# Kernel optimization log

Hardware: AMD Instinct MI355X
Metric: run time of the kernel (lower is better)

Reference implementation:

```python
import jax, jax.numpy as jnp
import numpy as np

# Qwen3-0.6B-like config; 4 equal-length requests flattened into [R*S, H]
L, R, S, H = 2, 4, 1024, 1024
NH, NKV, DH = 16, 8, 128
FF = 3072
EPS = 1e-6
THETA = 1e6
SCALE = 0.02  # weight init scale to keep activations sane


def setup_inputs() -> dict:
    key = jax.random.key(0)
    ks = jax.random.split(key, 8)
    return {
        "hidden_states": jax.random.normal(ks[0], (R * S, H), jnp.float32),
        "Wq": jax.random.normal(ks[1], (L, H, NH * DH), jnp.float32) * SCALE,
        "Wk": jax.random.normal(ks[2], (L, H, NKV * DH), jnp.float32) * SCALE,
        "Wv": jax.random.normal(ks[3], (L, H, NKV * DH), jnp.float32) * SCALE,
        "Wo": jax.random.normal(ks[4], (L, NH * DH, H), jnp.float32) * SCALE,
        "q_norm_w": jnp.ones((L, DH), jnp.float32),
        "k_norm_w": jnp.ones((L, DH), jnp.float32),
        "ln1_w": jnp.ones((L, H), jnp.float32),
        "ln2_w": jnp.ones((L, H), jnp.float32),
        "Wg": jax.random.normal(ks[5], (L, H, FF), jnp.float32) * SCALE,
        "Wu": jax.random.normal(ks[6], (L, H, FF), jnp.float32) * SCALE,
        "Wd": jax.random.normal(ks[7], (L, FF, H), jnp.float32) * SCALE,
        "final_norm_w": jnp.ones((H,), jnp.float32),
    }


def _rms(x, w):
    return x * jax.lax.rsqrt(jnp.mean(x * x, axis=-1, keepdims=True) + EPS) * w


def _rope_tables():
    inv_freq = 1.0 / (THETA ** (jnp.arange(0, DH, 2, dtype=jnp.float32) / DH))
    pos = jnp.arange(S, dtype=jnp.float32)  # per-request positions 0..S-1 (prefill)
    freqs = pos[:, None] * inv_freq[None, :]        # [S, DH/2]
    emb = jnp.concatenate([freqs, freqs], axis=-1)  # [S, DH]
    return jnp.cos(emb), jnp.sin(emb)


def _rotate_half(x):
    x1, x2 = jnp.split(x, 2, axis=-1)
    return jnp.concatenate([-x2, x1], axis=-1)


def _apply_rope(x, cos, sin):
    # x: [R, heads, S, DH]; cos/sin: [S, DH]
    c = cos[None, None]
    s = sin[None, None]
    return x * c + _rotate_half(x) * s


def reference(hidden_states, Wq, Wk, Wv, Wo, q_norm_w, k_norm_w, ln1_w, ln2_w,
              Wg, Wu, Wd, final_norm_w):
    cos, sin = _rope_tables()
    causal = jnp.tril(jnp.ones((S, S), dtype=bool))  # per-request causal mask
    neg = jnp.finfo(hidden_states.dtype).min
    scaling = 1.0 / jnp.sqrt(jnp.asarray(DH, hidden_states.dtype))

    x = hidden_states
    for l in range(L):
        # --- attention block ---
        residual = x
        h = _rms(x, ln1_w[l])                       # [R*S, H]
        q = (h @ Wq[l]).reshape(R, S, NH, DH)
        k = (h @ Wk[l]).reshape(R, S, NKV, DH)
        v = (h @ Wv[l]).reshape(R, S, NKV, DH)
        q = _rms(q, q_norm_w[l]).transpose(0, 2, 1, 3)   # [R, NH, S, DH]
        k = _rms(k, k_norm_w[l]).transpose(0, 2, 1, 3)   # [R, NKV, S, DH]
        v = v.transpose(0, 2, 1, 3)                      # [R, NKV, S, DH]
        q = _apply_rope(q, cos, sin)
        k = _apply_rope(k, cos, sin)
        # GQA: repeat KV heads
        rep = NH // NKV
        k = jnp.repeat(k, rep, axis=1)
        v = jnp.repeat(v, rep, axis=1)
        scores = jnp.einsum('rhqd,rhkd->rhqk', q, k) * scaling
        scores = jnp.where(causal[None, None], scores, neg)
        attn = jax.nn.softmax(scores, axis=-1)
        o = jnp.einsum('rhqk,rhkd->rhqd', attn, v)       # [R, NH, S, DH]
        o = o.transpose(0, 2, 1, 3).reshape(R * S, NH * DH)
        x = residual + o @ Wo[l]
        # --- MLP block ---
        residual = x
        h = _rms(x, ln2_w[l])
        x = residual + (jax.nn.silu(h @ Wg[l]) * (h @ Wu[l])) @ Wd[l]
    return _rms(x, final_norm_w)
```

## Files before the change

### kernel.cpp

```cpp
#include <hip/hip_runtime.h>
#include <hip/hip_bf16.h>

typedef __bf16 bf16;
typedef __bf16 bf16x8 __attribute__((ext_vector_type(8)));
typedef float f32x4 __attribute__((ext_vector_type(4)));

#define DEVINL __device__ __forceinline__

constexpr int L_ = 2, R_ = 4, S_ = 1024, H_ = 1024;
constexpr int NH_ = 16, NKV_ = 8, DH_ = 128;
constexpr int FF_ = 3072;
constexpr int T_ = R_ * S_;

DEVINL void gload16(const bf16* g, bf16* l) {
    __builtin_amdgcn_global_load_lds(
        (const __attribute__((address_space(1))) void*)g,
        (__attribute__((address_space(3))) void*)l, 16, 0, 0);
}

__global__ void rope_tables_kernel(float* __restrict__ cosb, float* __restrict__ sinb) {
    int s = blockIdx.x;
    int i = threadIdx.x;
    float inv = __expf(-(float)i * (1.0f / 64.0f) * 13.815510557964274f);
    float f = (float)s * inv;
    cosb[s * 64 + i] = cosf(f);
    sinb[s * 64 + i] = sinf(f);
}

template <bool OUT_BF16>
__global__ __launch_bounds__(256) void rmsnorm_kernel(const float* __restrict__ x,
                                                      const float* __restrict__ w,
                                                      void* __restrict__ out) {
    int row = blockIdx.x;
    const float* xr = x + (size_t)row * H_;
    int t = threadIdx.x;
    float v[4];
    float ss = 0.f;
#pragma unroll
    for (int j = 0; j < 4; ++j) {
        v[j] = xr[t + 256 * j];
        ss += v[j] * v[j];
    }
#pragma unroll
    for (int off = 32; off; off >>= 1) ss += __shfl_xor(ss, off);
    __shared__ float part[4];
    if ((t & 63) == 0) part[t >> 6] = ss;
    __syncthreads();
    ss = part[0] + part[1] + part[2] + part[3];
    float r = rsqrtf(ss * (1.0f / (float)H_) + 1e-6f);
#pragma unroll
    for (int j = 0; j < 4; ++j) {
        int c = t + 256 * j;
        float o = v[j] * r * w[c];
        if constexpr (OUT_BF16)
            ((bf16*)out)[(size_t)row * H_ + c] = (bf16)o;
        else
            ((float*)out)[(size_t)row * H_ + c] = o;
    }
}

__global__ __launch_bounds__(256) void transpose_cast_kernel(const float* __restrict__ in,
                                                             bf16* __restrict__ out,
                                                             int Rk, int Cn, int mode) {
    __shared__ float tile[32][33];
    int c0 = blockIdx.x * 32, r0 = blockIdx.y * 32;
    int t = threadIdx.x;
    int tc = t & 31, tr = t >> 5;
#pragma unroll
    for (int i = 0; i < 4; ++i) {
        int r = tr + i * 8;
        tile[r][tc] = in[(size_t)(r0 + r) * Cn + c0 + tc];
    }
    __syncthreads();
#pragma unroll
    for (int i = 0; i < 4; ++i) {
        int c = c0 + tr + i * 8;
        int n = (mode == 0) ? c : (((c >> 4) << 5) + ((mode == 2) ? 16 : 0) + (c & 15));
        out[(size_t)n * Rk + r0 + tc] = (bf16)tile[tc][tr + i * 8];
    }
}

__global__ __launch_bounds__(256) void vt_kernel(const bf16* __restrict__ qkv,
                                                 bf16* __restrict__ vt) {
    __shared__ bf16 tile[32][34];
    int s0 = blockIdx.x * 32, c0 = blockIdx.y * 32, r = blockIdx.z;
    int t = threadIdx.x, tc = t & 31, tr = t >> 5;
#pragma unroll
    for (int i = 0; i < 4; ++i) {
        int s = tr + i * 8;
        tile[s][tc] = qkv[(size_t)(r * 1024 + s0 + s) * 4096 + 3072 + c0 + tc];
    }
    __syncthreads();
#pragma unroll
    for (int i = 0; i < 4; ++i) {
        int c = tr + i * 8;
        vt[((size_t)(r * 1024 + c0 + c)) * 1024 + s0 + tc] = tile[tc][c];
    }
}

template <int EPI>
__global__ __launch_bounds__(512, 2) void gemmQ_kernel(const bf16* __restrict__ A,
                                                       const bf16* __restrict__ Bt,
                                                       void* __restrict__ out,
                                                       int M, int N, int K) {
    __shared__ bf16 lds[49152];
    const int NT = K >> 5;
    int nbm = M >> 8, nbn = N >> 8;
    int slice = nbn >> 3;
    int id = blockIdx.x;
    int xcd = id & 7, wi = id >> 3;
    int bm = (wi % nbm) << 8, bn = (xcd * slice + wi / nbm) << 8;
    int t = threadIdx.x, lane = t & 63, w = t >> 6;
    int wm = w >> 2, wn = w & 3;
    int hi = lane >> 4, f = lane & 15;

    int srow = t >> 2;
    int ssc = (t & 3) ^ ((srow >> 1) & 3);
    const bf16* a0 = A + (size_t)(bm + srow) * K + (ssc << 3);
    const bf16* a1 = A + (size_t)(bm + 128 + srow) * K + (ssc << 3);
    const bf16* b0 = Bt + (size_t)(bn + srow) * K + (ssc << 3);
    const bf16* b1 = Bt + (size_t)(bn + 128 + srow) * K + (ssc << 3);

    f32x4 acc[8][4] = {};

    auto stage = [&](int tt, int sb) {
        gload16(a0 + tt * 32, lds + sb * 8192 + w * 512);
        gload16(a1 + tt * 32, lds + sb * 8192 + 4096 + w * 512);
        gload16(b0 + tt * 32, lds + 24576 + sb * 8192 + w * 512);
        gload16(b1 + tt * 32, lds + 24576 + sb * 8192 + 4096 + w * 512);
    };

    stage(0, 0);
    stage(1, 1);
    asm volatile("s_waitcnt vmcnt(4)" ::: "memory");
    __builtin_amdgcn_s_barrier();

    int cb = 0;
    for (int tau = 0; tau < NT; ++tau) {
        const bf16* aB = lds + cb * 8192;
        const bf16* bB = lds + 24576 + cb * 8192;
        if (tau + 2 < NT) stage(tau + 2, (cb == 0) ? 2 : cb - 1);
        bf16x8 af[8], bfv[4];
#pragma unroll
        for (int mf = 0; mf < 8; ++mf) {
            int row = wm * 128 + mf * 16 + f;
            af[mf] = *(const bf16x8*)(aB + row * 32 + ((hi ^ ((row >> 1) & 3)) << 3));
        }
#pragma unroll
        for (int nf = 0; nf < 4; ++nf) {
            int row = wn * 64 + nf * 16 + f;
            bfv[nf] = *(const bf16x8*)(bB + row * 32 + ((hi ^ ((row >> 1) & 3)) << 3));
        }
        __builtin_amdgcn_s_setprio(1);
#pragma unroll
        for (int mf = 0; mf < 8; ++mf)
#pragma unroll
            for (int nf = 0; nf < 4; ++nf)
                acc[mf][nf] = __builtin_amdgcn_mfma_f32_16x16x32_bf16(af[mf], bfv[nf],
                                                                      acc[mf][nf], 0, 0, 0);
        __builtin_amdgcn_s_setprio(0);
        if (tau < NT - 2)
            asm volatile("s_waitcnt vmcnt(4)" ::: "memory");
        else
            asm volatile("s_waitcnt vmcnt(0)" ::: "memory");
        __builtin_amdgcn_s_barrier();
        cb = (cb == 2) ? 0 : cb + 1;
    }

    int rb = bm + wm * 128 + hi * 4;
    int cb2 = bn + wn * 64 + f;
#pragma unroll
    for (int mf = 0; mf < 8; ++mf)
#pragma unroll
        for (int nf = 0; nf < 4; ++nf)
#pragma unroll
            for (int g = 0; g < 4; ++g)
                ((bf16*)out)[(size_t)(rb + mf * 16 + g) * N + cb2 + nf * 16] =
                    (bf16)acc[mf][nf][g];
}

template <int EPI>
__global__ __launch_bounds__(512, 4) void gemmP_kernel(const bf16* __restrict__ A,
                                                       const bf16* __restrict__ Bt,
                                                       void* __restrict__ out,
                                                       int M, int N, int K) {
    __shared__ bf16 lds[36864];
    const int NT = K >> 5;
    int nbm = M >> 7, nbn = N >> 8;
    int slice = nbn >> 3;
    int id = blockIdx.x;
    int xcd = id & 7, wi = id >> 3;
    int bm = (wi % nbm) << 7, bn = (xcd * slice + wi / nbm) << 8;
    int t = threadIdx.x, lane = t & 63, w = t >> 6;
    int wm = w >> 2, wn = w & 3;
    int hi = lane >> 4, f = lane & 15;

    int srow = t >> 2;
    int ssc = (t & 3) ^ ((srow >> 1) & 3);
    const bf16* aSrc = A + (size_t)(bm + srow) * K + (ssc << 3);
    const bf16* b0Src = Bt + (size_t)(bn + srow) * K + (ssc << 3);
    const bf16* b1Src = Bt + (size_t)(bn + 128 + srow) * K + (ssc << 3);

    f32x4 acc[4][4] = {};

    auto stage = [&](int tt, int sb) {
        gload16(aSrc + tt * 32, lds + sb * 4096 + w * 512);
        gload16(b0Src + tt * 32, lds + 12288 + sb * 8192 + w * 512);
        gload16(b1Src + tt * 32, lds + 12288 + sb * 8192 + 4096 + w * 512);
    };

    stage(0, 0);
    stage(1, 1);
    asm volatile("s_waitcnt vmcnt(3)" ::: "memory");
    __builtin_amdgcn_s_barrier();

    int cb = 0;
    for (int tau = 0; tau < NT; ++tau) {
        const bf16* aB = lds + cb * 4096;
        const bf16* bB = lds + 12288 + cb * 8192;
        if (tau + 2 < NT) stage(tau + 2, (cb == 0) ? 2 : cb - 1);
        bf16x8 af[4], bfv[4];
#pragma unroll
        for (int mf = 0; mf < 4; ++mf) {
            int row = wm * 64 + mf * 16 + f;
            af[mf] = *(const bf16x8*)(aB + row * 32 + ((hi ^ ((row >> 1) & 3)) << 3));
        }
#pragma unroll
        for (int nf = 0; nf < 4; ++nf) {
            int row = wn * 64 + nf * 16 + f;
            bfv[nf] = *(const bf16x8*)(bB + row * 32 + ((hi ^ ((row >> 1) & 3)) << 3));
        }
        __builtin_amdgcn_s_setprio(1);
#pragma unroll
        for (int mf = 0; mf < 4; ++mf)
#pragma unroll
            for (int nf = 0; nf < 4; ++nf)
                acc[mf][nf] = __builtin_amdgcn_mfma_f32_16x16x32_bf16(af[mf], bfv[nf],
                                                                      acc[mf][nf], 0, 0, 0);
        __builtin_amdgcn_s_setprio(0);
        if (tau < NT - 2)
            asm volatile("s_waitcnt vmcnt(3)" ::: "memory");
        else
            asm volatile("s_waitcnt vmcnt(0)" ::: "memory");
        __builtin_amdgcn_s_barrier();
        cb = (cb == 2) ? 0 : cb + 1;
    }

    int rb = bm + wm * 64 + hi * 4;
#pragma unroll
    for (int mf = 0; mf < 4; ++mf) {
        if constexpr (EPI == 5) {
#pragma unroll
            for (int p = 0; p < 2; ++p) {
                int col = ((bn + wn * 64) >> 1) + p * 16 + f;
#pragma unroll
                for (int g = 0; g < 4; ++g) {
                    float gv = acc[mf][2 * p][g], uv = acc[mf][2 * p + 1][g];
                    float sv = gv / (1.0f + __expf(-gv));
                    ((bf16*)out)[(size_t)(rb + mf * 16 + g) * (N / 2) + col] = (bf16)(sv * uv);
                }
            }
        } else {
            int cb2 = bn + wn * 64 + f;
#pragma unroll
            for (int nf = 0; nf < 4; ++nf)
#pragma unroll
                for (int g = 0; g < 4; ++g)
                    ((bf16*)out)[(size_t)(rb + mf * 16 + g) * N + cb2 + nf * 16] =
                        (bf16)acc[mf][nf][g];
        }
    }
}

template <int EPI, int BM>
__global__ __launch_bounds__(256) void gemm_kernel(const bf16* __restrict__ A,
                                                   const bf16* __restrict__ Bt,
                                                   void* __restrict__ out,
                                                   const float* __restrict__ res,
                                                   int M, int N, int K) {
    constexpr int MF = BM / 32;
    __shared__ bf16 Al[BM * 32];
    __shared__ bf16 Bl[128 * 32];
    int gx = gridDim.x;
    int nbm = gridDim.y;
    int id = blockIdx.y * gx + blockIdx.x;
    int slice = gx >> 3;
    int xcd = id & 7, wi = id >> 3;
    int bm = (wi % nbm) * BM, bn = (xcd * slice + wi / nbm) * 128;
    int t = threadIdx.x;
    int lane = t & 63, w = t >> 6;
    int wr = w >> 1, wc = w & 1;
    f32x4 acc[MF][4] = {};

    int srow = t >> 2, scol = (t & 3) * 8;
    const bf16* Ap = A + (size_t)(bm + srow) * K + scol;
    const bf16* Bp = Bt + (size_t)(bn + srow) * K + scol;
    bf16* Adst = Al + w * 512;
    bf16* Bdst = Bl + w * 512;

    int kl = (lane >> 4) * 8;
    int rm = wr * (BM / 2) + (lane & 15);
    int rn = wc * 64 + (lane & 15);

    for (int k0 = 0; k0 < K; k0 += 32) {
        __syncthreads();
        gload16(Ap, Adst);
        if constexpr (BM == 128) gload16(Ap + (size_t)64 * K, Adst + 2048);
        gload16(Bp, Bdst);
        gload16(Bp + (size_t)64 * K, Bdst + 2048);
        Ap += 32;
        Bp += 32;
        __syncthreads();
        bf16x8 af[MF], bfv[4];
#pragma unroll
        for (int m = 0; m < MF; ++m) af[m] = *(const bf16x8*)(Al + (rm + m * 16) * 32 + kl);
#pragma unroll
        for (int n = 0; n < 4; ++n) bfv[n] = *(const bf16x8*)(Bl + (rn + n * 16) * 32 + kl);
#pragma unroll
        for (int m = 0; m < MF; ++m)
#pragma unroll
            for (int n = 0; n < 4; ++n)
                acc[m][n] = __builtin_amdgcn_mfma_f32_16x16x32_bf16(af[m], bfv[n], acc[m][n], 0, 0, 0);
    }

    int f = lane & 15;
    int rbase = bm + wr * (BM / 2) + ((lane >> 4) << 2);
    int cbase = bn + wc * 64 + f;
#pragma unroll
    for (int m = 0; m < MF; ++m) {
#pragma unroll
        for (int n = 0; n < 4; ++n) {
#pragma unroll
            for (int g = 0; g < 4; ++g) {
                int row = rbase + m * 16 + g;
                size_t idx = (size_t)row * N + cbase + n * 16;
                ((float*)out)[idx] = acc[m][n][g] + res[idx];
            }
        }
    }
}

DEVINL void head_norm_rope(const bf16* __restrict__ src, const float* __restrict__ w,
                           const float* __restrict__ cosb, const float* __restrict__ sinb,
                           int s, int ln, bf16* __restrict__ dst) {
    float x0 = (float)src[ln], x1 = (float)src[ln + 32];
    float x2 = (float)src[ln + 64], x3 = (float)src[ln + 96];
    float ss = x0 * x0 + x1 * x1 + x2 * x2 + x3 * x3;
#pragma unroll
    for (int off = 16; off; off >>= 1) ss += __shfl_xor(ss, off);
    float rr = rsqrtf(ss * (1.0f / 128.0f) + 1e-6f);
    float n0 = x0 * rr * w[ln], n1 = x1 * rr * w[ln + 32];
    float n2 = x2 * rr * w[ln + 64], n3 = x3 * rr * w[ln + 96];
    float c0 = cosb[s * 64 + ln], c1 = cosb[s * 64 + ln + 32];
    float s0 = sinb[s * 64 + ln], s1 = sinb[s * 64 + ln + 32];
    dst[ln] = (bf16)(n0 * c0 - n2 * s0);
    dst[ln + 32] = (bf16)(n1 * c1 - n3 * s1);
    dst[ln + 64] = (bf16)(n2 * c0 + n0 * s0);
    dst[ln + 96] = (bf16)(n3 * c1 + n1 * s1);
}

__global__ __launch_bounds__(256) void qkv_post_kernel(const bf16* __restrict__ qkv,
                                                       const float* __restrict__ qw,
                                                       const float* __restrict__ kw,
                                                       const float* __restrict__ cosb,
                                                       const float* __restrict__ sinb,
                                                       bf16* __restrict__ qo,
                                                       bf16* __restrict__ ko) {
    int tok = blockIdx.x;
    int r = tok >> 10, s = tok & 1023;
    int t = threadIdx.x;
    int g = t >> 5;
    int ln = t & 31;
    const bf16* row = qkv + (size_t)tok * 4096;
#pragma unroll
    for (int hh = 0; hh < 2; ++hh) {
        int h = g + hh * 8;
        head_norm_rope(row + h * 128, qw, cosb, sinb, s, ln,
                       qo + ((size_t)(r * NH_ + h) * S_ + s) * 128);
    }
    head_norm_rope(row + 2048 + g * 128, kw, cosb, sinb, s, ln,
                   ko + ((size_t)(r * NKV_ + g) * S_ + s) * 128);
}

__global__ __launch_bounds__(256, 2) void flash_kernel(const bf16* __restrict__ q,
                                                       const bf16* __restrict__ k,
                                                       const bf16* __restrict__ vt,
                                                       bf16* __restrict__ out) {
    __shared__ bf16 Kl[64 * 128];
    __shared__ bf16 Vl[128 * 64];
    __shared__ bf16 Pl[4][32][72];
    int bid = blockIdx.x;
    int grp = bid & 63, slot = bid >> 6;
    int strip = (slot < 4) ? (7 - slot) : (slot - 4);
    int h = 2 * (grp & 7) + ((grp >> 3) & 1);
    int r = grp >> 4;
    int kvh = h >> 1;

    int t = threadIdx.x, lane = t & 63, w = t >> 6;
    int arow = lane & 15, hi = lane >> 4;
    int a7 = arow & 7;
    int grow = hi * 4;
    int qbase = strip * 128 + w * 32;

    const bf16* qp = q + ((size_t)(r * NH_ + h) * S_ + qbase) * 128;
    bf16x8 qf[2][4];
#pragma unroll
    for (int m = 0; m < 2; ++m)
#pragma unroll
        for (int kc = 0; kc < 4; ++kc)
            qf[m][kc] = *(const bf16x8*)(qp + (size_t)(m * 16 + arow) * 128 + kc * 32 + hi * 8);

    const bf16* kp = k + (size_t)(r * NKV_ + kvh) * S_ * 128;
    const bf16* vp = vt + (size_t)(r * NKV_ + kvh) * 128 * S_;

    int krow0 = t >> 4, kc16 = t & 15;
    int vrow0 = t >> 3, vc16 = t & 7;

    f32x4 ao[2][8] = {};
    float mrow[2][4], lrow[2][4];
#pragma unroll
    for (int m = 0; m < 2; ++m)
#pragma unroll
        for (int g = 0; g < 4; ++g) { mrow[m][g] = -1e30f; lrow[m][g] = 0.f; }
    const float scale = 0.08838834764831845f;

    int nt = 2 * (strip + 1);
    bf16x8 krs[4], vrs[4];
#pragma unroll
    for (int i = 0; i < 4; ++i)
        krs[i] = *(const bf16x8*)(kp + (size_t)(krow0 + 16 * i) * 128 + kc16 * 8);
#pragma unroll
    for (int i = 0; i < 4; ++i)
        vrs[i] = *(const bf16x8*)(vp + (size_t)(vrow0 + 32 * i) * S_ + vc16 * 8);

    for (int it = 0; it < nt; ++it) {
        int kv0 = it * 64;
        __syncthreads();
#pragma unroll
        for (int i = 0; i < 4; ++i) {
            int row = krow0 + 16 * i;
            *(bf16x8*)(&Kl[row * 128 + ((kc16 ^ (row & 7)) * 8)]) = krs[i];
        }
#pragma unroll
        for (int i = 0; i < 4; ++i) {
            int row = vrow0 + 32 * i;
            *(bf16x8*)(&Vl[row * 64 + ((vc16 ^ (row & 7)) * 8)]) = vrs[i];
        }
        __syncthreads();
        if (it + 1 < nt) {
            int kvn = kv0 + 64;
#pragma unroll
            for (int i = 0; i < 4; ++i)
                krs[i] = *(const bf16x8*)(kp + (size_t)(kvn + krow0 + 16 * i) * 128 + kc16 * 8);
#pragma unroll
            for (int i = 0; i < 4; ++i)
                vrs[i] = *(const bf16x8*)(vp + (size_t)(vrow0 + 32 * i) * S_ + kvn + vc16 * 8);
        }
        f32x4 sc[2][4];
#pragma unroll
        for (int m = 0; m < 2; ++m)
#pragma unroll
            for (int n = 0; n < 4; ++n) sc[m][n] = (f32x4){0.f, 0.f, 0.f, 0.f};
#pragma unroll
        for (int n = 0; n < 4; ++n) {
            int krw = n * 16 + arow;
#pragma unroll
            for (int kc = 0; kc < 4; ++kc) {
                bf16x8 kf = *(const bf16x8*)(&Kl[krw * 128 + (((kc * 4 + hi) ^ a7) * 8)]);
                sc[0][n] = __builtin_amdgcn_mfma_f32_16x16x32_bf16(qf[0][kc], kf, sc[0][n], 0, 0, 0);
                sc[1][n] = __builtin_amdgcn_mfma_f32_16x16x32_bf16(qf[1][kc], kf, sc[1][n], 0, 0, 0);
            }
        }
#pragma unroll
        for (int m = 0; m < 2; ++m) {
            float pm[4][4];
            bool msk = (kv0 + 64 > qbase + m * 16);
#pragma unroll
            for (int n = 0; n < 4; ++n)
#pragma unroll
                for (int g = 0; g < 4; ++g) {
                    float sval = sc[m][n][g] * scale;
                    if (msk && (kv0 + n * 16 + arow > qbase + m * 16 + grow + g)) sval = -1e30f;
                    pm[n][g] = sval;
                }
            float mx[4], sf[4], rs[4];
#pragma unroll
            for (int g = 0; g < 4; ++g)
                mx[g] = fmaxf(fmaxf(pm[0][g], pm[1][g]), fmaxf(pm[2][g], pm[3][g]));
#pragma unroll
            for (int off = 8; off; off >>= 1)
#pragma unroll
                for (int g = 0; g < 4; ++g) mx[g] = fmaxf(mx[g], __shfl_xor(mx[g], off));
#pragma unroll
            for (int g = 0; g < 4; ++g) {
                float mnew = fmaxf(mrow[m][g], mx[g]);
                sf[g] = __expf(mrow[m][g] - mnew);
                mrow[m][g] = mnew;
            }
#pragma unroll
            for (int n = 0; n < 4; ++n)
#pragma unroll
                for (int g = 0; g < 4; ++g) pm[n][g] = __expf(pm[n][g] - mrow[m][g]);
#pragma unroll
            for (int g = 0; g < 4; ++g) rs[g] = pm[0][g] + pm[1][g] + pm[2][g] + pm[3][g];
#pragma unroll
            for (int off = 8; off; off >>= 1)
#pragma unroll
                for (int g = 0; g < 4; ++g) rs[g] += __shfl_xor(rs[g], off);
#pragma unroll
            for (int g = 0; g < 4; ++g) lrow[m][g] = lrow[m][g] * sf[g] + rs[g];
#pragma unroll
            for (int c = 0; c < 8; ++c)
#pragma unroll
                for (int g = 0; g < 4; ++g) ao[m][c][g] *= sf[g];
#pragma unroll
            for (int n = 0; n < 4; ++n)
#pragma unroll
                for (int g = 0; g < 4; ++g)
                    Pl[w][m * 16 + grow + g][n * 16 + arow] = (bf16)pm[n][g];
        }
        bf16x8 pf[2][2];
#pragma unroll
        for (int m = 0; m < 2; ++m)
#pragma unroll
            for (int ks = 0; ks < 2; ++ks)
                pf[m][ks] = *(const bf16x8*)(&Pl[w][m * 16 + arow][ks * 32 + hi * 8]);
#pragma unroll
        for (int c = 0; c < 8; ++c) {
            int vrw = c * 16 + arow;
#pragma unroll
            for (int ks = 0; ks < 2; ++ks) {
                bf16x8 vf = *(const bf16x8*)(&Vl[vrw * 64 + (((ks * 4 + hi) ^ a7) * 8)]);
                ao[0][c] = __builtin_amdgcn_mfma_f32_16x16x32_bf16(pf[0][ks], vf, ao[0][c], 0, 0, 0);
                ao[1][c] = __builtin_amdgcn_mfma_f32_16x16x32_bf16(pf[1][ks], vf, ao[1][c], 0, 0, 0);
            }
        }
    }
#pragma unroll
    for (int m = 0; m < 2; ++m)
#pragma unroll
        for (int c = 0; c < 8; ++c)
#pragma unroll
            for (int g = 0; g < 4; ++g) {
                int rq = qbase + m * 16 + grow + g;
                out[(size_t)(r * S_ + rq) * 2048 + h * 128 + c * 16 + arow] =
                    (bf16)(ao[m][c][g] / lrow[m][g]);
            }
}

extern "C" void kernel_launch(void* const* d_in, const int* in_sizes, int n_in,
                              void* d_out, int out_size, void* d_ws, size_t ws_size,
                              hipStream_t stream) {
    const float* hidden = (const float*)d_in[0];
    const float* Wq = (const float*)d_in[1];
    const float* Wk = (const float*)d_in[2];
    const float* Wv = (const float*)d_in[3];
    const float* Wo = (const float*)d_in[4];
    const float* qnw = (const float*)d_in[5];
    const float* knw = (const float*)d_in[6];
    const float* ln1 = (const float*)d_in[7];
    const float* ln2 = (const float*)d_in[8];
    const float* Wg = (const float*)d_in[9];
    const float* Wu = (const float*)d_in[10];
    const float* Wd = (const float*)d_in[11];
    const float* fnw = (const float*)d_in[12];
    float* out = (float*)d_out;

    char* ws = (char*)d_ws;
    size_t off = 0;
    auto alloc = [&](size_t bytes) -> char* {
        char* p = ws + off;
        off += (bytes + 255) & ~(size_t)255;
        return p;
    };
    float* cosb = (float*)alloc((size_t)S_ * 64 * 4);
    float* sinb = (float*)alloc((size_t)S_ * 64 * 4);
    float* x_ws = (float*)alloc((size_t)T_ * H_ * 4);
    bf16* hbuf = (bf16*)alloc((size_t)T_ * H_ * 2);
    bf16* qkv = (bf16*)alloc((size_t)T_ * 4096 * 2);
    bf16* act = qkv;
    bf16* qb = (bf16*)alloc((size_t)R_ * NH_ * S_ * 128 * 2);
    bf16* kb = (bf16*)alloc((size_t)R_ * NKV_ * S_ * 128 * 2);
    bf16* vtb = (bf16*)alloc((size_t)R_ * NKV_ * 128 * S_ * 2);
    bf16* attn = (bf16*)alloc((size_t)T_ * 2048 * 2);
    bf16* wqkv_t = (bf16*)alloc((size_t)4096 * 1024 * 2);
    bf16* wo_t = (bf16*)alloc((size_t)1024 * 2048 * 2);
    bf16* wgu_t = (bf16*)alloc((size_t)6144 * 1024 * 2);
    bf16* wd_t = (bf16*)alloc((size_t)1024 * 3072 * 2);

    rope_tables_kernel<<<S_, 64, 0, stream>>>(cosb, sinb);

    const float* xin = hidden;
    for (int l = 0; l < L_; ++l) {
        transpose_cast_kernel<<<dim3(2048 / 32, 1024 / 32), 256, 0, stream>>>(
            Wq + (size_t)l * H_ * 2048, wqkv_t, 1024, 2048, 0);
        transpose_cast_kernel<<<dim3(1024 / 32, 1024 / 32), 256, 0, stream>>>(
            Wk + (size_t)l * H_ * 1024, wqkv_t + (size_t)2048 * 1024, 1024, 1024, 0);
        transpose_cast_kernel<<<dim3(1024 / 32, 1024 / 32), 256, 0, stream>>>(
            Wv + (size_t)l * H_ * 1024, wqkv_t + (size_t)3072 * 1024, 1024, 1024, 0);
        transpose_cast_kernel<<<dim3(1024 / 32, 2048 / 32), 256, 0, stream>>>(
            Wo + (size_t)l * 2048 * 1024, wo_t, 2048, 1024, 0);
        transpose_cast_kernel<<<dim3(3072 / 32, 1024 / 32), 256, 0, stream>>>(
            Wg + (size_t)l * H_ * 3072, wgu_t, 1024, 3072, 1);
        transpose_cast_kernel<<<dim3(3072 / 32, 1024 / 32), 256, 0, stream>>>(
            Wu + (size_t)l * H_ * 3072, wgu_t, 1024, 3072, 2);
        transpose_cast_kernel<<<dim3(1024 / 32, 3072 / 32), 256, 0, stream>>>(
            Wd + (size_t)l * 3072 * 1024, wd_t, 3072, 1024, 0);

        rmsnorm_kernel<true><<<T_, 256, 0, stream>>>(xin, ln1 + (size_t)l * H_, hbuf);
        gemmQ_kernel<1><<<256, 512, 0, stream>>>(hbuf, wqkv_t, qkv, 4096, 4096, 1024);
        qkv_post_kernel<<<T_, 256, 0, stream>>>(qkv, qnw + (size_t)l * 128, knw + (size_t)l * 128,
                                                cosb, sinb, qb, kb);
        vt_kernel<<<dim3(32, 32, 4), 256, 0, stream>>>(qkv, vtb);
        flash_kernel<<<512, 256, 0, stream>>>(qb, kb, vtb, attn);
        gemm_kernel<4, 64><<<dim3(8, 64), 256, 0, stream>>>(attn, wo_t, x_ws, xin,
                                                            4096, 1024, 2048);
        rmsnorm_kernel<true><<<T_, 256, 0, stream>>>(x_ws, ln2 + (size_t)l * H_, hbuf);
        gemmP_kernel<5><<<768, 512, 0, stream>>>(hbuf, wgu_t, act, 4096, 6144, 1024);
        gemm_kernel<4, 64><<<dim3(8, 64), 256, 0, stream>>>(act, wd_t, x_ws, x_ws,
                                                            4096, 1024, 3072);
        xin = x_ws;
    }
    rmsnorm_kernel<false><<<T_, 256, 0, stream>>>(x_ws, fnw, out);
}
```

Before: 616.2 us.

## Rewrite residual GEMM with triple-buffered LDS pipeline, XOR swizzle, and K=64 tiles

Replaces the simple single-buffer residual GEMM used for the O-projection and down-projection with a kernel that triple-buffers 64-wide K tiles in LDS. Global-to-LDS loads for the tile two steps ahead are issued while the current tile is computed, with vmcnt waits replacing the double syncthreads per step. An XOR swizzle avoids LDS bank conflicts, and setprio raises priority around the MFMA block. It uses about 72KB of LDS per block with a 2-block occupancy hint, which may limit how many blocks fit on a CU.

```diff
diff --git a/kernel.cpp b/kernel.cpp
--- a/kernel.cpp
+++ b/kernel.cpp
@@ -272,72 +272,96 @@
     }
 }
 
-template <int EPI, int BM>
-__global__ __launch_bounds__(256) void gemm_kernel(const bf16* __restrict__ A,
-                                                   const bf16* __restrict__ Bt,
-                                                   void* __restrict__ out,
-                                                   const float* __restrict__ res,
-                                                   int M, int N, int K) {
-    constexpr int MF = BM / 32;
-    __shared__ bf16 Al[BM * 32];
-    __shared__ bf16 Bl[128 * 32];
-    int gx = gridDim.x;
-    int nbm = gridDim.y;
-    int id = blockIdx.y * gx + blockIdx.x;
-    int slice = gx >> 3;
+template <int EPI>
+__global__ __launch_bounds__(256, 2) void gemmD_kernel(const bf16* __restrict__ A,
+                                                       const bf16* __restrict__ Bt,
+                                                       void* __restrict__ out,
+                                                       const float* __restrict__ res,
+                                                       int M, int N, int K) {
+    __shared__ bf16 lds[36864];
+    const int NT = K >> 6;
+    int nbm = M >> 6;
+    int id = blockIdx.x;
     int xcd = id & 7, wi = id >> 3;
-    int bm = (wi % nbm) * BM, bn = (xcd * slice + wi / nbm) * 128;
-    int t = threadIdx.x;
-    int lane = t & 63, w = t >> 6;
-    int wr = w >> 1, wc = w & 1;
-    f32x4 acc[MF][4] = {};
-
-    int srow = t >> 2, scol = (t & 3) * 8;
-    const bf16* Ap = A + (size_t)(bm + srow) * K + scol;
-    const bf16* Bp = Bt + (size_t)(bn + srow) * K + scol;
-    bf16* Adst = Al + w * 512;
-    bf16* Bdst = Bl + w * 512;
-
-    int kl = (lane >> 4) * 8;
-    int rm = wr * (BM / 2) + (lane & 15);
-    int rn = wc * 64 + (lane & 15);
-
-    for (int k0 = 0; k0 < K; k0 += 32) {
-        __syncthreads();
-        gload16(Ap, Adst);
-        if constexpr (BM == 128) gload16(Ap + (size_t)64 * K, Adst + 2048);
-        gload16(Bp, Bdst);
-        gload16(Bp + (size_t)64 * K, Bdst + 2048);
-        Ap += 32;
-        Bp += 32;
-        __syncthreads();
-        bf16x8 af[MF], bfv[4];
-#pragma unroll
-        for (int m = 0; m < MF; ++m) af[m] = *(const bf16x8*)(Al + (rm + m * 16) * 32 + kl);
-#pragma unroll
-        for (int n = 0; n < 4; ++n) bfv[n] = *(const bf16x8*)(Bl + (rn + n * 16) * 32 + kl);
-#pragma unroll
-        for (int m = 0; m < MF; ++m)
-#pragma unroll
-            for (int n = 0; n < 4; ++n)
-                acc[m][n] = __builtin_amdgcn_mfma_f32_16x16x32_bf16(af[m], bfv[n], acc[m][n], 0, 0, 0);
-    }
-
-    int f = lane & 15;
-    int rbase = bm + wr * (BM / 2) + ((lane >> 4) << 2);
-    int cbase = bn + wc * 64 + f;
-#pragma unroll
-    for (int m = 0; m < MF; ++m) {
-#pragma unroll
-        for (int n = 0; n < 4; ++n) {
+    int bm = (wi % nbm) << 6, bn = xcd << 7;
+    int t = threadIdx.x, lane = t & 63, w = t >> 6;
+    int wm = w >> 1, wn = w & 1;
+    int hi = lane >> 4, f = lane & 15;
+
+    int ar0 = t >> 3, ac0 = t & 7;
+    const bf16* aS0 = A + (size_t)(bm + ar0) * K + (((ac0 ^ (ar0 & 7)) & 7) << 3);
+    const bf16* aS1 = A + (size_t)(bm + 32 + ar0) * K + (((ac0 ^ ((ar0 + 32) & 7)) & 7) << 3);
+    const bf16* bS[4];
+#pragma unroll
+    for (int j = 0; j < 4; ++j) {
+        int row = j * 32 + ar0;
+        bS[j] = Bt + (size_t)(bn + row) * K + (((ac0 ^ (row & 7)) & 7) << 3);
+    }
+
+    f32x4 acc[2][4] = {};
+
+    auto stage = [&](int tt, int sb) {
+        gload16(aS0 + tt * 64, lds + sb * 4096 + w * 512);
+        gload16(aS1 + tt * 64, lds + sb * 4096 + 2048 + w * 512);
+#pragma unroll
+        for (int j = 0; j < 4; ++j)
+            gload16(bS[j] + tt * 64, lds + 12288 + sb * 8192 + j * 2048 + w * 512);
+    };
+
+    stage(0, 0);
+    stage(1, 1);
+    asm volatile("s_waitcnt vmcnt(6)" ::: "memory");
+    __builtin_amdgcn_s_barrier();
+
+    int cb = 0;
+    for (int tau = 0; tau < NT; ++tau) {
+        const bf16* aB = lds + cb * 4096;
+        const bf16* bB = lds + 12288 + cb * 8192;
+        if (tau + 2 < NT) stage(tau + 2, (cb == 0) ? 2 : cb - 1);
+        bf16x8 af[2][2], bfv[2][4];
+#pragma unroll
+        for (int kh = 0; kh < 2; ++kh) {
+            int q = kh * 4 + hi;
+#pragma unroll
+            for (int mf = 0; mf < 2; ++mf) {
+                int row = wm * 32 + mf * 16 + f;
+                af[kh][mf] = *(const bf16x8*)(aB + row * 64 + ((q ^ (row & 7)) << 3));
+            }
+#pragma unroll
+            for (int nf = 0; nf < 4; ++nf) {
+                int row = wn * 64 + nf * 16 + f;
+                bfv[kh][nf] = *(const bf16x8*)(bB + row * 64 + ((q ^ (row & 7)) << 3));
+            }
+        }
+        __builtin_amdgcn_s_setprio(1);
+#pragma unroll
+        for (int kh = 0; kh < 2; ++kh)
+#pragma unroll
+            for (int mf = 0; mf < 2; ++mf)
+#pragma unroll
+                for (int nf = 0; nf < 4; ++nf)
+                    acc[mf][nf] = __builtin_amdgcn_mfma_f32_16x16x32_bf16(
+                        af[kh][mf], bfv[kh][nf], acc[mf][nf], 0, 0, 0);
+        __builtin_amdgcn_s_setprio(0);
+        if (tau < NT - 2)
+            asm volatile("s_waitcnt vmcnt(6)" ::: "memory");
+        else
+            asm volatile("s_waitcnt vmcnt(0)" ::: "memory");
+        __builtin_amdgcn_s_barrier();
+        cb = (cb == 2) ? 0 : cb + 1;
+    }
+
+    int rb = bm + wm * 32 + hi * 4;
+    int cb2 = bn + wn * 64 + f;
+#pragma unroll
+    for (int mf = 0; mf < 2; ++mf)
+#pragma unroll
+        for (int nf = 0; nf < 4; ++nf)
 #pragma unroll
             for (int g = 0; g < 4; ++g) {
-                int row = rbase + m * 16 + g;
-                size_t idx = (size_t)row * N + cbase + n * 16;
-                ((float*)out)[idx] = acc[m][n][g] + res[idx];
-            }
-        }
-    }
+                size_t idx = (size_t)(rb + mf * 16 + g) * N + cb2 + nf * 16;
+                ((float*)out)[idx] = acc[mf][nf][g] + res[idx];
+            }
 }
 
 DEVINL void head_norm_rope(const bf16* __restrict__ src, const float* __restrict__ w,
@@ -613,12 +637,10 @@
                                                 cosb, sinb, qb, kb);
         vt_kernel<<<dim3(32, 32, 4), 256, 0, stream>>>(qkv, vtb);
         flash_kernel<<<512, 256, 0, stream>>>(qb, kb, vtb, attn);
-        gemm_kernel<4, 64><<<dim3(8, 64), 256, 0, stream>>>(attn, wo_t, x_ws, xin,
-                                                            4096, 1024, 2048);
+        gemmD_kernel<4><<<512, 256, 0, stream>>>(attn, wo_t, x_ws, xin, 4096, 1024, 2048);
         rmsnorm_kernel<true><<<T_, 256, 0, stream>>>(x_ws, ln2 + (size_t)l * H_, hbuf);
         gemmP_kernel<5><<<768, 512, 0, stream>>>(hbuf, wgu_t, act, 4096, 6144, 1024);
-        gemm_kernel<4, 64><<<dim3(8, 64), 256, 0, stream>>>(act, wd_t, x_ws, x_ws,
-                                                            4096, 1024, 3072);
+        gemmD_kernel<4><<<512, 256, 0, stream>>>(act, wd_t, x_ws, x_ws, 4096, 1024, 3072);
         xin = x_ws;
     }
     rmsnorm_kernel<false><<<T_, 256, 0, stream>>>(x_ws, fnw, out);
```

Measured after the change: 541.5 us. -12.1%, faster.
